# Optimization experiments

Measured on AMD Instinct MI355X. Metric: run time of the kernel, lower is better.

## Reference

```python
import jax, jax.numpy as jnp
import numpy as np

VOL = 128
FACTOR = 0.5 * VOL
N = 262144
LAT = 16
B = 8


def setup_inputs() -> dict:
    key = jax.random.key(0)
    ks = jax.random.split(key, 10)
    x = jax.random.normal(ks[0], (B, LAT), jnp.float32)
    inds = jax.random.randint(ks[1], (N, 3), 1, 126, dtype=jnp.int32)
    reference_values = jax.random.normal(ks[2], (N,), jnp.float32)
    # SIREN first layer: U(-1/in, 1/in)
    W0 = jax.random.uniform(ks[3], (LAT, 8), jnp.float32, -1.0 / LAT, 1.0 / LAT)
    b0 = jnp.zeros((8,), jnp.float32)
    # SIREN hidden layers (4 residual layers): U(-sqrt(6/in), sqrt(6/in))
    lim_h = float(np.sqrt(6.0 / 8.0))
    Wh = jax.random.uniform(ks[4], (4, 8, 8), jnp.float32, -lim_h, lim_h)
    bh = jnp.zeros((4, 8), jnp.float32)
    # final glorot-uniform layer: 8 -> 4N
    lim_f = float(np.sqrt(6.0 / (8.0 + 4.0 * N)))
    Wf = jax.random.uniform(ks[5], (8, 4 * N), jnp.float32, -lim_f, lim_f)
    bf = jnp.zeros((4 * N,), jnp.float32)
    return {"x": x, "W0": W0, "b0": b0, "Wh": Wh, "bh": bh, "Wf": Wf,
            "bf": bf, "reference_values": reference_values, "inds": inds}


def _siren_mlp(x, W0, b0, Wh, bh, Wf, bf):
    bf16 = jnp.bfloat16
    h = jnp.sin(30.0 * (x.astype(bf16) @ W0.astype(bf16) + b0.astype(bf16)))
    for i in range(Wh.shape[0]):  # 4 residual sine layers, 8-wide
        h = h + jnp.sin(h @ Wh[i].astype(bf16) + bh[i].astype(bf16))
    return h.astype(jnp.float32) @ Wf + bf  # [B, 4N], final layer in fp32


def reference(x, W0, b0, Wh, bh, Wf, bf, reference_values, inds):
    Bn = x.shape[0]
    out = _siren_mlp(x, W0, b0, Wh, bh, Wf, bf).reshape(Bn, N, 4)
    delta_coords, delta_values = out[..., :3], out[..., 3]
    # coords = stack(z,y,x reversed) normalized to [-1,1)
    coords_norm = (jnp.stack([inds[:, 2], inds[:, 1], inds[:, 0]], axis=1)
                   .astype(jnp.float32) - FACTOR) / FACTOR  # [N,3]
    values = reference_values + delta_values                 # [B,N]
    coords = FACTOR * (coords_norm[None] + delta_coords) + FACTOR  # [B,N,3]
    bposf = jnp.floor(coords)
    bposi = bposf.astype(jnp.int32)
    f = coords - bposf
    fx, fy, fz = f[..., 0], f[..., 1], f[..., 2]
    gx, gy, gz = 1.0 - fx, 1.0 - fy, 1.0 - fz
    # 8 trilinear weights, in the original concat order
    w = jnp.stack([gx * gy * gz, fx * gy * gz, gx * fy * gz, gx * gy * fz,
                   gx * fy * fz, fx * gy * fz, fx * fy * gz, fx * fy * fz],
                  axis=1)                                    # [B,8,N]
    bamp = (values[:, None, :] * w).reshape(Bn, 8 * N)
    offs = jnp.array([[0, 0, 0], [1, 0, 0], [0, 1, 0], [0, 0, 1],
                      [0, 1, 1], [1, 0, 1], [1, 1, 0], [1, 1, 1]], jnp.int32)
    bpos = (bposi[:, None, :, :] + offs[None, :, None, :]).reshape(Bn, 8 * N, 3)

    def scatter(pos, amp):
        return jnp.zeros((VOL, VOL, VOL), jnp.float32).at[
            pos[:, 2], pos[:, 1], pos[:, 0]].add(amp)

    grids = jax.vmap(scatter)(bpos, bamp)  # [B,128,128,128]
    return grids
```

## Files before the change

kernel.cpp:

```cpp
#include <hip/hip_runtime.h>
#include <math.h>

#define VOL   128
#define V2    (VOL*VOL)
#define V3    (VOL*VOL*VOL)
#define NPTS  262144
#define LATD  16
#define BATCH 8
#define FACTORF 64.0f
#define NBINS (VOL*VOL)
#define RZ 8
#define RY 8
#define NREG_TOTAL 2048
#define REGION_WGS 1280
#define FAR_CAP 8192

#define WS_HBUF    0u
#define WS_HIST    256u
#define WS_START   65792u
#define WS_RANK    131344u
#define WS_KEYS    1179920u
#define WS_CTRL    1704208u
#define WS_FARLIST 1704240u
#define WS_COORDS  1737008u
#define WS_FULL    35291440u

__device__ __forceinline__ float bf16r(float x) {
    unsigned u = __float_as_uint(x);
    u = (u + 0x7fffu + ((u >> 16) & 1u)) & 0xffff0000u;
    return __uint_as_float(u);
}

__global__ void mlp_kernel(const float* __restrict__ x,
                           const float* __restrict__ W0,
                           const float* __restrict__ b0,
                           const float* __restrict__ Wh,
                           const float* __restrict__ bh,
                           float* __restrict__ hout) {
    int b = threadIdx.x;
    if (b >= BATCH) return;
    float xb[LATD];
    #pragma unroll
    for (int i = 0; i < LATD; ++i) xb[i] = bf16r(x[b*LATD + i]);
    float h[8];
    #pragma unroll
    for (int j = 0; j < 8; ++j) {
        float acc = 0.f;
        #pragma unroll
        for (int i = 0; i < LATD; ++i) acc += xb[i] * bf16r(W0[i*8 + j]);
        float t = bf16r(acc);
        t = bf16r(t + bf16r(b0[j]));
        t = bf16r(30.0f * t);
        h[j] = bf16r(sinf(t));
    }
    for (int l = 0; l < 4; ++l) {
        float nh[8];
        #pragma unroll
        for (int j = 0; j < 8; ++j) {
            float acc = 0.f;
            #pragma unroll
            for (int r = 0; r < 8; ++r) acc += h[r] * bf16r(Wh[(l*8 + r)*8 + j]);
            float t = bf16r(acc);
            t = bf16r(t + bf16r(bh[l*8 + j]));
            float s = bf16r(sinf(t));
            nh[j] = bf16r(h[j] + s);
        }
        #pragma unroll
        for (int j = 0; j < 8; ++j) h[j] = nh[j];
    }
    #pragma unroll
    for (int j = 0; j < 8; ++j) hout[b*8 + j] = h[j];
}

__global__ __launch_bounds__(256) void hist_rank_kernel(const int* __restrict__ inds,
                                                        unsigned* __restrict__ hist,
                                                        unsigned* __restrict__ rank) {
    int n = blockIdx.x * 256 + threadIdx.x;
    if (n >= NPTS) return;
    rank[n] = atomicAdd(&hist[inds[n*3]*VOL + inds[n*3+1]], 1u);
}

__global__ __launch_bounds__(256) void scan_kernel(const unsigned* __restrict__ hist,
                                                   unsigned* __restrict__ binstart,
                                                   unsigned* __restrict__ ctrl) {
    __shared__ unsigned part[256];
    int t = threadIdx.x;
    const int CH = NBINS / 256;
    unsigned s = 0;
    for (int k = 0; k < CH; ++k) s += hist[t*CH + k];
    part[t] = s; __syncthreads();
    for (int off = 1; off < 256; off <<= 1) {
        unsigned v = (t >= off) ? part[t - off] : 0u;
        __syncthreads();
        part[t] += v;
        __syncthreads();
    }
    unsigned run = (t == 0) ? 0u : part[t - 1];
    for (int k = 0; k < CH; ++k) {
        int idx = t*CH + k;
        binstart[idx] = run;
        run += hist[idx];
    }
    if (t == 0) { binstart[NBINS] = NPTS; ctrl[0] = 0u; ctrl[1] = 0u; }
}

__global__ __launch_bounds__(256) void coords_kernel(
    const float* __restrict__ Wf, const float* __restrict__ bfv_g,
    const float* __restrict__ rv, const int* __restrict__ inds,
    const float* __restrict__ hbuf, const unsigned* __restrict__ binstart,
    const unsigned* __restrict__ rank, unsigned short* __restrict__ keys,
    unsigned* __restrict__ ctrl, unsigned* __restrict__ farlist,
    float4* __restrict__ coords_s)
{
    __shared__ float hs[64];
    if (threadIdx.x < 64) hs[threadIdx.x] = hbuf[threadIdx.x];
    __syncthreads();
    int n = blockIdx.x * 256 + threadIdx.x;
    if (n >= NPTS) return;
    int iz = inds[n*3], iy = inds[n*3+1], ix = inds[n*3+2];
    float cnx = ((float)ix - FACTORF) / FACTORF;
    float cny = ((float)iy - FACTORF) / FACTORF;
    float cnz = ((float)iz - FACTORF) / FACTORF;
    float val0 = rv[n];
    float4 bfv = ((const float4*)bfv_g)[n];
    float4 wf[8];
    #pragma unroll
    for (int r = 0; r < 8; ++r)
        wf[r] = ((const float4*)(Wf + (size_t)r * 4 * NPTS))[n];
    unsigned pos = binstart[iz*VOL + iy] + rank[n];
    keys[pos] = (unsigned short)((iz << 7) | iy);
    #pragma unroll
    for (int b = 0; b < BATCH; ++b) {
        float o0 = bfv.x, o1 = bfv.y, o2 = bfv.z, o3 = bfv.w;
        #pragma unroll
        for (int r = 0; r < 8; ++r) {
            float hv = hs[b*8 + r];
            o0 = fmaf(hv, wf[r].x, o0);
            o1 = fmaf(hv, wf[r].y, o1);
            o2 = fmaf(hv, wf[r].z, o2);
            o3 = fmaf(hv, wf[r].w, o3);
        }
        float4 c;
        c.x = FACTORF * (cnx + o0) + FACTORF;
        c.y = FACTORF * (cny + o1) + FACTORF;
        c.z = FACTORF * (cnz + o2) + FACTORF;
        c.w = val0 + o3;
        coords_s[(size_t)b * NPTS + pos] = c;
        int bz = (int)floorf(c.z), by = (int)floorf(c.y);
        bool nearzy = ((unsigned)(bz - iz + 2) <= 4u) &&
                      ((unsigned)(by - iy + 2) <= 4u);
        if (!nearzy) {
            unsigned fp = atomicAdd(&ctrl[0], 1u);
            if (fp < FAR_CAP) farlist[fp] = (pos << 3) | (unsigned)b;
        }
    }
}

__global__ __launch_bounds__(256) void region_kernel(
    const float4* __restrict__ coords_s, const unsigned short* __restrict__ keys,
    const unsigned* __restrict__ binstart, unsigned* __restrict__ ctrl,
    float* __restrict__ out)
{
    __shared__ float tile[RZ*RY*VOL];
    __shared__ int reg_s;
    int tid = threadIdx.x;

    const int ox[8] = {0,1,0,0,0,1,1,1};
    const int oy[8] = {0,0,1,0,1,0,1,1};
    const int oz[8] = {0,0,0,1,1,1,0,1};

    for (;;) {
        __syncthreads();
        if (tid == 0) reg_s = (int)atomicAdd(&ctrl[1], 1u);
        __syncthreads();
        int reg = reg_s;
        if (reg >= NREG_TOTAL) return;
        int b   = reg >> 8;
        int rid = reg & 255;
        int z0 = (rid >> 4) * RZ, y0 = (rid & 15) * RY;

        for (int i = tid; i < RZ*RY*VOL; i += 256) tile[i] = 0.f;
        __syncthreads();

        int ylo = y0 - 3, yhi = y0 + RY + 2;
        int sA0, sA1, sB0, sB1;
        if (ylo < 0)        { sA0 = ylo + VOL; sA1 = VOL; sB0 = 0; sB1 = yhi; }
        else if (yhi > VOL) { sA0 = ylo; sA1 = VOL; sB0 = 0; sB1 = yhi - VOL; }
        else                { sA0 = ylo; sA1 = yhi; sB0 = 0; sB1 = 0; }

        const float4* cb = coords_s + (size_t)b * NPTS;

        for (int zr = z0 - 3; zr < z0 + RZ + 2; ++zr) {
            int zz = (zr + VOL) & (VOL-1);
            int base = zz * VOL;
            for (int sg = 0; sg < 2; ++sg) {
                int a  = sg ? sB0 : sA0;
                int e2 = sg ? sB1 : sA1;
                if (a >= e2) continue;
                unsigned s = binstart[base + a];
                unsigned e = binstart[base + e2];
                for (unsigned i = s + tid; i < e; i += 256) {
                    unsigned kv = keys[i];
                    int piz = (int)(kv >> 7), piy = (int)(kv & 127);
                    float4 c = cb[i];
                    float fxf = floorf(c.x), fyf = floorf(c.y), fzf = floorf(c.z);
                    int bx = (int)fxf, by = (int)fyf, bz = (int)fzf;
                    bool nearzy = ((unsigned)(bz - piz + 2) <= 4u) &&
                                  ((unsigned)(by - piy + 2) <= 4u);
                    if (!nearzy) continue;
                    float fx = c.x - fxf, fy = c.y - fyf, fz = c.z - fzf;
                    float gx = 1.f - fx, gy = 1.f - fy, gz = 1.f - fz;
                    float val = c.w;
                    float w[8] = {gx*gy*gz, fx*gy*gz, gx*fy*gz, gx*gy*fz,
                                  gx*fy*fz, fx*gy*fz, fx*fy*gz, fx*fy*fz};
                    #pragma unroll
                    for (int o = 0; o < 8; ++o) {
                        int Z = (bz + oz[o]) & 127, dz = Z - z0;
                        if ((unsigned)dz >= RZ) continue;
                        int Y = (by + oy[o]) & 127, dy = Y - y0;
                        if ((unsigned)dy >= RY) continue;
                        int X = (bx + ox[o]) & 127;
                        atomicAdd(&tile[(dz << 10) + (dy << 7) + X], val * w[o]);
                    }
                }
            }
        }
        __syncthreads();
        size_t ob = (size_t)b * V3;
        for (int i = tid; i < RZ*RY*VOL; i += 256) {
            int lz = i >> 10, ly = (i >> 7) & (RY-1), lx = i & 127;
            out[ob + (size_t)(z0+lz)*V2 + (y0+ly)*VOL + lx] = tile[i];
        }
    }
}

__global__ __launch_bounds__(256) void far_kernel(
    const float4* __restrict__ coords_s, const unsigned* __restrict__ ctrl,
    const unsigned* __restrict__ farlist, float* __restrict__ out)
{
    unsigned cnt = ctrl[0];
    if (cnt > FAR_CAP) cnt = FAR_CAP;
    const int ox[8] = {0,1,0,0,0,1,1,1};
    const int oy[8] = {0,0,1,0,1,0,1,1};
    const int oz[8] = {0,0,0,1,1,1,0,1};
    for (unsigned idx = blockIdx.x * 256 + threadIdx.x; idx < cnt;
         idx += gridDim.x * 256) {
        unsigned e = farlist[idx];
        unsigned pos = e >> 3;
        int b = (int)(e & 7u);
        float4 c = coords_s[(size_t)b * NPTS + pos];
        float fxf = floorf(c.x), fyf = floorf(c.y), fzf = floorf(c.z);
        int bx = (int)fxf, by = (int)fyf, bz = (int)fzf;
        float fx = c.x - fxf, fy = c.y - fyf, fz = c.z - fzf;
        float gx = 1.f - fx, gy = 1.f - fy, gz = 1.f - fz;
        float val = c.w;
        float w[8] = {gx*gy*gz, fx*gy*gz, gx*fy*gz, gx*gy*fz,
                      gx*fy*fz, fx*gy*fz, fx*fy*gz, fx*fy*fz};
        float* ob = out + (size_t)b * V3;
        #pragma unroll
        for (int o = 0; o < 8; ++o) {
            int Z = (bz + oz[o]) & 127;
            int Y = (by + oy[o]) & 127;
            int X = (bx + ox[o]) & 127;
            atomicAdd(ob + (size_t)Z*V2 + Y*VOL + X, val * w[o]);
        }
    }
}

__global__ __launch_bounds__(256) void scatter_fallback(
    const float* __restrict__ Wf, const float* __restrict__ bfv_g,
    const float* __restrict__ rv, const int* __restrict__ inds,
    const float* __restrict__ hbuf, float* __restrict__ out)
{
    __shared__ float hs[BATCH*8];
    if (threadIdx.x < BATCH*8) hs[threadIdx.x] = hbuf[threadIdx.x];
    __syncthreads();
    int n = blockIdx.x * blockDim.x + threadIdx.x;
    if (n >= NPTS) return;
    int iz = inds[n*3 + 0], iy = inds[n*3 + 1], ix = inds[n*3 + 2];
    float cnx = ((float)ix - FACTORF) / FACTORF;
    float cny = ((float)iy - FACTORF) / FACTORF;
    float cnz = ((float)iz - FACTORF) / FACTORF;
    float val0 = rv[n];
    float4 bfv = ((const float4*)bfv_g)[n];
    float4 wf[8];
    #pragma unroll
    for (int r = 0; r < 8; ++r)
        wf[r] = ((const float4*)(Wf + (size_t)r * 4 * NPTS))[n];
    static const int offs[8][3] = {{0,0,0},{1,0,0},{0,1,0},{0,0,1},
                                   {0,1,1},{1,0,1},{1,1,0},{1,1,1}};
    #pragma unroll
    for (int b = 0; b < BATCH; ++b) {
        float o0 = bfv.x, o1 = bfv.y, o2 = bfv.z, o3 = bfv.w;
        #pragma unroll
        for (int r = 0; r < 8; ++r) {
            float hv = hs[b*8 + r];
            o0 = fmaf(hv, wf[r].x, o0);
            o1 = fmaf(hv, wf[r].y, o1);
            o2 = fmaf(hv, wf[r].z, o2);
            o3 = fmaf(hv, wf[r].w, o3);
        }
        float cx = FACTORF * (cnx + o0) + FACTORF;
        float cy = FACTORF * (cny + o1) + FACTORF;
        float cz = FACTORF * (cnz + o2) + FACTORF;
        float val = val0 + o3;
        float fxf = floorf(cx), fyf = floorf(cy), fzf = floorf(cz);
        int bx = (int)fxf, by = (int)fyf, bz = (int)fzf;
        float fx = cx - fxf, fy = cy - fyf, fz = cz - fzf;
        float gx = 1.f - fx, gy = 1.f - fy, gz = 1.f - fz;
        float w[8] = {gx*gy*gz, fx*gy*gz, gx*fy*gz, gx*gy*fz,
                      gx*fy*fz, fx*gy*fz, fx*fy*gz, fx*fy*fz};
        float* ob = out + (size_t)b * V3;
        #pragma unroll
        for (int o = 0; o < 8; ++o) {
            int X = (bx + offs[o][0]) & (VOL-1);
            int Y = (by + offs[o][1]) & (VOL-1);
            int Z = (bz + offs[o][2]) & (VOL-1);
            atomicAdd(ob + (size_t)Z*V2 + Y*VOL + X, val * w[o]);
        }
    }
}

extern "C" void kernel_launch(void* const* d_in, const int* in_sizes, int n_in,
                              void* d_out, int out_size, void* d_ws, size_t ws_size,
                              hipStream_t stream) {
    const float* x    = (const float*)d_in[0];
    const float* W0   = (const float*)d_in[1];
    const float* b0   = (const float*)d_in[2];
    const float* Wh   = (const float*)d_in[3];
    const float* bh   = (const float*)d_in[4];
    const float* Wf   = (const float*)d_in[5];
    const float* bf   = (const float*)d_in[6];
    const float* rv   = (const float*)d_in[7];
    const int*   inds = (const int*)d_in[8];
    float* out = (float*)d_out;
    char*  ws  = (char*)d_ws;

    float*          hbuf     = (float*)(ws + WS_HBUF);
    unsigned*       hist     = (unsigned*)(ws + WS_HIST);
    unsigned*       binstart = (unsigned*)(ws + WS_START);
    unsigned*       rank     = (unsigned*)(ws + WS_RANK);
    unsigned short* keys     = (unsigned short*)(ws + WS_KEYS);
    unsigned*       ctrl     = (unsigned*)(ws + WS_CTRL);
    unsigned*       farlist  = (unsigned*)(ws + WS_FARLIST);
    float4*         coords_s = (float4*)(ws + WS_COORDS);

    mlp_kernel<<<1, 64, 0, stream>>>(x, W0, b0, Wh, bh, hbuf);

    if (ws_size >= (size_t)WS_FULL) {
        hipMemsetAsync(hist, 0, NBINS*4, stream);
        hist_rank_kernel<<<NPTS/256, 256, 0, stream>>>(inds, hist, rank);
        scan_kernel<<<1, 256, 0, stream>>>(hist, binstart, ctrl);
        coords_kernel<<<NPTS/256, 256, 0, stream>>>(Wf, bf, rv, inds, hbuf,
                                                    binstart, rank, keys,
                                                    ctrl, farlist, coords_s);
        region_kernel<<<REGION_WGS, 256, 0, stream>>>(coords_s, keys, binstart,
                                                      ctrl, out);
        far_kernel<<<8, 256, 0, stream>>>(coords_s, ctrl, farlist, out);
    } else {
        hipMemsetAsync(d_out, 0, (size_t)out_size * sizeof(float), stream);
        scatter_fallback<<<NPTS/256, 256, 0, stream>>>(Wf, bf, rv, inds, hbuf, out);
    }
}
```

Baseline: 200.8 us.

## Use static one-region-per-block grid with flattened segment loop and unrolled loads

Replaces the persistent atomic work-queue region kernel with one workgroup per smaller region (RY halved to 4), launching 4096 blocks. Each block precomputes the 26 bin segments of its halo into shared memory and walks them as one flattened index space, issuing four independent loads per thread before the scatter arithmetic. This is meant to remove per-segment loop overhead and idle lanes on short segments, and to raise memory-level parallelism and occupancy. In exchange the halo overlap per block grows, so more points are read and filtered redundantly.

```diff
diff --git a/kernel.cpp b/kernel.cpp
--- a/kernel.cpp
+++ b/kernel.cpp
@@ -10,9 +10,8 @@
 #define FACTORF 64.0f
 #define NBINS (VOL*VOL)
 #define RZ 8
-#define RY 8
-#define NREG_TOTAL 2048
-#define REGION_WGS 1280
+#define RY 4
+#define REG_PER_B ((VOL/RZ)*(VOL/RY))
 #define FAR_CAP 8192
 
 #define WS_HBUF    0u
@@ -158,79 +157,93 @@
 
 __global__ __launch_bounds__(256) void region_kernel(
     const float4* __restrict__ coords_s, const unsigned short* __restrict__ keys,
-    const unsigned* __restrict__ binstart, unsigned* __restrict__ ctrl,
-    float* __restrict__ out)
+    const unsigned* __restrict__ binstart, float* __restrict__ out)
 {
     __shared__ float tile[RZ*RY*VOL];
-    __shared__ int reg_s;
+    __shared__ unsigned rstart[26], rcnt[26], rcum[27];
     int tid = threadIdx.x;
+    int b   = blockIdx.x >> 9;
+    int rid = blockIdx.x & (REG_PER_B - 1);
+    int z0 = (rid >> 5) * RZ, y0 = (rid & 31) * RY;
+
+    for (int i = tid; i < RZ*RY*VOL; i += 256) tile[i] = 0.f;
+
+    if (tid < 13) {
+        int zr = z0 - 3 + tid;
+        int zz = (zr + VOL) & (VOL-1);
+        int base = zz * VOL;
+        int ylo = y0 - 3, yhi = y0 + RY + 2;
+        int a0, a1, b0, b1;
+        if (ylo < 0)        { a0 = ylo + VOL; a1 = VOL; b0 = 0; b1 = yhi; }
+        else if (yhi > VOL) { a0 = ylo; a1 = VOL; b0 = 0; b1 = yhi - VOL; }
+        else                { a0 = ylo; a1 = yhi; b0 = 0; b1 = 0; }
+        unsigned sA = binstart[base + a0];
+        rstart[tid*2]   = sA;
+        rcnt[tid*2]     = binstart[base + a1] - sA;
+        unsigned sB = binstart[base + b0];
+        rstart[tid*2+1] = sB;
+        rcnt[tid*2+1]   = (b1 > b0) ? (binstart[base + b1] - sB) : 0u;
+    }
+    __syncthreads();
+    if (tid == 0) {
+        unsigned run = 0;
+        #pragma unroll
+        for (int r = 0; r < 26; ++r) { rcum[r] = run; run += rcnt[r]; }
+        rcum[26] = run;
+    }
+    __syncthreads();
 
     const int ox[8] = {0,1,0,0,0,1,1,1};
     const int oy[8] = {0,0,1,0,1,0,1,1};
     const int oz[8] = {0,0,0,1,1,1,0,1};
-
-    for (;;) {
-        __syncthreads();
-        if (tid == 0) reg_s = (int)atomicAdd(&ctrl[1], 1u);
-        __syncthreads();
-        int reg = reg_s;
-        if (reg >= NREG_TOTAL) return;
-        int b   = reg >> 8;
-        int rid = reg & 255;
-        int z0 = (rid >> 4) * RZ, y0 = (rid & 15) * RY;
-
-        for (int i = tid; i < RZ*RY*VOL; i += 256) tile[i] = 0.f;
-        __syncthreads();
-
-        int ylo = y0 - 3, yhi = y0 + RY + 2;
-        int sA0, sA1, sB0, sB1;
-        if (ylo < 0)        { sA0 = ylo + VOL; sA1 = VOL; sB0 = 0; sB1 = yhi; }
-        else if (yhi > VOL) { sA0 = ylo; sA1 = VOL; sB0 = 0; sB1 = yhi - VOL; }
-        else                { sA0 = ylo; sA1 = yhi; sB0 = 0; sB1 = 0; }
-
-        const float4* cb = coords_s + (size_t)b * NPTS;
-
-        for (int zr = z0 - 3; zr < z0 + RZ + 2; ++zr) {
-            int zz = (zr + VOL) & (VOL-1);
-            int base = zz * VOL;
-            for (int sg = 0; sg < 2; ++sg) {
-                int a  = sg ? sB0 : sA0;
-                int e2 = sg ? sB1 : sA1;
-                if (a >= e2) continue;
-                unsigned s = binstart[base + a];
-                unsigned e = binstart[base + e2];
-                for (unsigned i = s + tid; i < e; i += 256) {
-                    unsigned kv = keys[i];
-                    int piz = (int)(kv >> 7), piy = (int)(kv & 127);
-                    float4 c = cb[i];
-                    float fxf = floorf(c.x), fyf = floorf(c.y), fzf = floorf(c.z);
-                    int bx = (int)fxf, by = (int)fyf, bz = (int)fzf;
-                    bool nearzy = ((unsigned)(bz - piz + 2) <= 4u) &&
-                                  ((unsigned)(by - piy + 2) <= 4u);
-                    if (!nearzy) continue;
-                    float fx = c.x - fxf, fy = c.y - fyf, fz = c.z - fzf;
-                    float gx = 1.f - fx, gy = 1.f - fy, gz = 1.f - fz;
-                    float val = c.w;
-                    float w[8] = {gx*gy*gz, fx*gy*gz, gx*fy*gz, gx*gy*fz,
-                                  gx*fy*fz, fx*gy*fz, fx*fy*gz, fx*fy*fz};
-                    #pragma unroll
-                    for (int o = 0; o < 8; ++o) {
-                        int Z = (bz + oz[o]) & 127, dz = Z - z0;
-                        if ((unsigned)dz >= RZ) continue;
-                        int Y = (by + oy[o]) & 127, dy = Y - y0;
-                        if ((unsigned)dy >= RY) continue;
-                        int X = (bx + ox[o]) & 127;
-                        atomicAdd(&tile[(dz << 10) + (dy << 7) + X], val * w[o]);
-                    }
-                }
+    const float4* cb = coords_s + (size_t)b * NPTS;
+
+    unsigned total = rcum[26];
+    int r = 0;
+    for (unsigned f = tid; f < total; f += 1024) {
+        float4 c[4]; unsigned kk[4]; bool v[4];
+        #pragma unroll
+        for (int u = 0; u < 4; ++u) {
+            unsigned fu = f + (unsigned)u * 256u;
+            v[u] = fu < total;
+            if (v[u]) {
+                while (fu >= rcum[r+1]) ++r;
+                unsigned j = rstart[r] + (fu - rcum[r]);
+                c[u]  = cb[j];
+                kk[u] = keys[j];
             }
         }
-        __syncthreads();
-        size_t ob = (size_t)b * V3;
-        for (int i = tid; i < RZ*RY*VOL; i += 256) {
-            int lz = i >> 10, ly = (i >> 7) & (RY-1), lx = i & 127;
-            out[ob + (size_t)(z0+lz)*V2 + (y0+ly)*VOL + lx] = tile[i];
-        }
+        #pragma unroll
+        for (int u = 0; u < 4; ++u) {
+            if (!v[u]) continue;
+            int piz = (int)(kk[u] >> 7), piy = (int)(kk[u] & 127u);
+            float4 cc = c[u];
+            float fxf = floorf(cc.x), fyf = floorf(cc.y), fzf = floorf(cc.z);
+            int bx = (int)fxf, by = (int)fyf, bz = (int)fzf;
+            bool nearzy = ((unsigned)(bz - piz + 2) <= 4u) &&
+                          ((unsigned)(by - piy + 2) <= 4u);
+            if (!nearzy) continue;
+            float fx = cc.x - fxf, fy = cc.y - fyf, fz = cc.z - fzf;
+            float gx = 1.f - fx, gy = 1.f - fy, gz = 1.f - fz;
+            float val = cc.w;
+            float w[8] = {gx*gy*gz, fx*gy*gz, gx*fy*gz, gx*gy*fz,
+                          gx*fy*fz, fx*gy*fz, fx*fy*gz, fx*fy*fz};
+            #pragma unroll
+            for (int o = 0; o < 8; ++o) {
+                int Z = (bz + oz[o]) & 127, dz = Z - z0;
+                if ((unsigned)dz >= RZ) continue;
+                int Y = (by + oy[o]) & 127, dy = Y - y0;
+                if ((unsigned)dy >= RY) continue;
+                int X = (bx + ox[o]) & 127;
+                atomicAdd(&tile[(dz << 9) + (dy << 7) + X], val * w[o]);
+            }
+        }
+    }
+    __syncthreads();
+    size_t ob = (size_t)b * V3;
+    for (int i = tid; i < RZ*RY*VOL; i += 256) {
+        int lz = i >> 9, ly = (i >> 7) & (RY-1), lx = i & 127;
+        out[ob + (size_t)(z0+lz)*V2 + (y0+ly)*VOL + lx] = tile[i];
     }
 }
 
@@ -354,8 +367,8 @@
         coords_kernel<<<NPTS/256, 256, 0, stream>>>(Wf, bf, rv, inds, hbuf,
                                                     binstart, rank, keys,
                                                     ctrl, farlist, coords_s);
-        region_kernel<<<REGION_WGS, 256, 0, stream>>>(coords_s, keys, binstart,
-                                                      ctrl, out);
+        region_kernel<<<REG_PER_B*BATCH, 256, 0, stream>>>(coords_s, keys,
+                                                           binstart, out);
         far_kernel<<<8, 256, 0, stream>>>(coords_s, ctrl, farlist, out);
     } else {
         hipMemsetAsync(d_out, 0, (size_t)out_size * sizeof(float), stream);
```

Result: faster. 179.9 us (-10.4%).

## Compress sorted per-point coords to fixed-point ushort4 and flatten region scheduling

Applied to the files above, without the earlier changes.

The coords kernel now stores each near point as a 64-bit record: fixed-point x, y and z offsets relative to the point's bin, plus an fp16 value. This replaces the float4 record and the separate keys array. Far points are written as full float4 records into a dedicated buffer, with the batch index folded into z. The region kernel drops its atomic work-queue for a static one-block-per-region grid. Each block builds a shared-memory index table over its 13x13 halo bins and processes eight points per thread per iteration to raise memory-level parallelism. This roughly halves intermediate traffic but adds quantisation error in coordinates (1/256 in x) and in values (fp16), which may break accuracy tolerance.

```diff
diff --git a/kernel.cpp b/kernel.cpp
--- a/kernel.cpp
+++ b/kernel.cpp
@@ -1,5 +1,7 @@
 #include <hip/hip_runtime.h>
+#include <hip/hip_fp16.h>
 #include <math.h>
+#include <string.h>
 
 #define VOL   128
 #define V2    (VOL*VOL)
@@ -11,24 +13,33 @@
 #define NBINS (VOL*VOL)
 #define RZ 8
 #define RY 8
-#define NREG_TOTAL 2048
-#define REGION_WGS 1280
+#define HALO 13
+#define NRANGE (HALO*HALO)
+#define TBL_CAP 4096
 #define FAR_CAP 8192
 
-#define WS_HBUF    0u
-#define WS_HIST    256u
-#define WS_START   65792u
-#define WS_RANK    131344u
-#define WS_KEYS    1179920u
-#define WS_CTRL    1704208u
-#define WS_FARLIST 1704240u
-#define WS_COORDS  1737008u
-#define WS_FULL    35291440u
+#define WS_HBUF   0u
+#define WS_HIST   256u
+#define WS_START  65792u
+#define WS_RANK   131344u
+#define WS_CTRL   1179920u
+#define WS_FARBUF 1179952u
+#define WS_COORDC 1311024u
+#define WS_FULL   18088240u
 
 __device__ __forceinline__ float bf16r(float x) {
     unsigned u = __float_as_uint(x);
     u = (u + 0x7fffu + ((u >> 16) & 1u)) & 0xffff0000u;
     return __uint_as_float(u);
+}
+__device__ __forceinline__ unsigned short f16bits(float v) {
+    __half h = __float2half_rn(v);
+    unsigned short us; memcpy(&us, &h, 2);
+    return us;
+}
+__device__ __forceinline__ float f16val(unsigned short us) {
+    __half h; memcpy(&h, &us, 2);
+    return __half2float(h);
 }
 
 __global__ void mlp_kernel(const float* __restrict__ x,
@@ -108,9 +119,9 @@
     const float* __restrict__ Wf, const float* __restrict__ bfv_g,
     const float* __restrict__ rv, const int* __restrict__ inds,
     const float* __restrict__ hbuf, const unsigned* __restrict__ binstart,
-    const unsigned* __restrict__ rank, unsigned short* __restrict__ keys,
-    unsigned* __restrict__ ctrl, unsigned* __restrict__ farlist,
-    float4* __restrict__ coords_s)
+    const unsigned* __restrict__ rank,
+    unsigned* __restrict__ ctrl, float4* __restrict__ farbuf,
+    ushort4* __restrict__ coords_c)
 {
     __shared__ float hs[64];
     if (threadIdx.x < 64) hs[threadIdx.x] = hbuf[threadIdx.x];
@@ -128,7 +139,6 @@
     for (int r = 0; r < 8; ++r)
         wf[r] = ((const float4*)(Wf + (size_t)r * 4 * NPTS))[n];
     unsigned pos = binstart[iz*VOL + iy] + rank[n];
-    keys[pos] = (unsigned short)((iz << 7) | iy);
     #pragma unroll
     for (int b = 0; b < BATCH; ++b) {
         float o0 = bfv.x, o1 = bfv.y, o2 = bfv.z, o3 = bfv.w;
@@ -140,103 +150,135 @@
             o2 = fmaf(hv, wf[r].z, o2);
             o3 = fmaf(hv, wf[r].w, o3);
         }
-        float4 c;
-        c.x = FACTORF * (cnx + o0) + FACTORF;
-        c.y = FACTORF * (cny + o1) + FACTORF;
-        c.z = FACTORF * (cnz + o2) + FACTORF;
-        c.w = val0 + o3;
-        coords_s[(size_t)b * NPTS + pos] = c;
-        int bz = (int)floorf(c.z), by = (int)floorf(c.y);
+        float cx = FACTORF * (cnx + o0) + FACTORF;
+        float cy = FACTORF * (cny + o1) + FACTORF;
+        float cz = FACTORF * (cnz + o2) + FACTORF;
+        float val = val0 + o3;
+        int bz = (int)floorf(cz), by = (int)floorf(cy);
         bool nearzy = ((unsigned)(bz - iz + 2) <= 4u) &&
                       ((unsigned)(by - iy + 2) <= 4u);
-        if (!nearzy) {
+        ushort4 e;
+        if (nearzy) {
+            e.x = (unsigned short)fminf(fmaxf(fmaf(cx + 8.f, 256.f, 0.5f), 0.f), 65535.f);
+            e.y = (unsigned short)fminf(fmaf(cy - (float)iy + 2.f, 8192.f, 0.5f), 40959.f);
+            e.z = (unsigned short)fminf(fmaf(cz - (float)iz + 2.f, 8192.f, 0.5f), 40959.f);
+            e.w = f16bits(val);
+        } else {
+            e.x = 0; e.y = 0xFFFFu; e.z = 0; e.w = 0;
             unsigned fp = atomicAdd(&ctrl[0], 1u);
-            if (fp < FAR_CAP) farlist[fp] = (pos << 3) | (unsigned)b;
-        }
+            if (fp < FAR_CAP)
+                farbuf[fp] = make_float4(cx, cy, cz + 256.0f * (float)b, val);
+        }
+        coords_c[(size_t)b * NPTS + pos] = e;
     }
 }
 
 __global__ __launch_bounds__(256) void region_kernel(
-    const float4* __restrict__ coords_s, const unsigned short* __restrict__ keys,
-    const unsigned* __restrict__ binstart, unsigned* __restrict__ ctrl,
-    float* __restrict__ out)
+    const ushort4* __restrict__ coords_c,
+    const unsigned* __restrict__ binstart, float* __restrict__ out)
 {
     __shared__ float tile[RZ*RY*VOL];
-    __shared__ int reg_s;
+    __shared__ unsigned tbl[TBL_CAP];
+    __shared__ unsigned rcum[NRANGE+1];
+    __shared__ int rbase[NRANGE];
     int tid = threadIdx.x;
-
+    int b   = blockIdx.x >> 8;
+    int rid = blockIdx.x & 255;
+    int z0 = (rid >> 4) * RZ, y0 = (rid & 15) * RY;
+
+    for (int i = tid; i < RZ*RY*VOL; i += 256) tile[i] = 0.f;
+
+    unsigned rs = 0;
+    if (tid < NRANGE) {
+        int zi = tid / HALO, yi = tid - zi * HALO;
+        int zz = (z0 - 3 + zi) & (VOL-1);
+        int yy = (y0 - 3 + yi) & (VOL-1);
+        int base = zz * VOL + yy;
+        rs = binstart[base];
+        rcum[tid+1] = binstart[base+1] - rs;
+    }
+    if (tid == 0) rcum[0] = 0u;
+    __syncthreads();
+    for (int off = 1; off < NRANGE; off <<= 1) {
+        unsigned v = 0u;
+        if (tid < NRANGE && tid >= off) v = rcum[tid+1-off];
+        __syncthreads();
+        if (tid < NRANGE && tid >= off) rcum[tid+1] += v;
+        __syncthreads();
+    }
+    if (tid < NRANGE) rbase[tid] = (int)rs - (int)rcum[tid];
+    __syncthreads();
+
+    unsigned total = rcum[NRANGE];
+    const ushort4* cb = coords_c + (size_t)b * NPTS;
     const int ox[8] = {0,1,0,0,0,1,1,1};
     const int oy[8] = {0,0,1,0,1,0,1,1};
     const int oz[8] = {0,0,0,1,1,1,0,1};
 
-    for (;;) {
-        __syncthreads();
-        if (tid == 0) reg_s = (int)atomicAdd(&ctrl[1], 1u);
-        __syncthreads();
-        int reg = reg_s;
-        if (reg >= NREG_TOTAL) return;
-        int b   = reg >> 8;
-        int rid = reg & 255;
-        int z0 = (rid >> 4) * RZ, y0 = (rid & 15) * RY;
-
-        for (int i = tid; i < RZ*RY*VOL; i += 256) tile[i] = 0.f;
-        __syncthreads();
-
-        int ylo = y0 - 3, yhi = y0 + RY + 2;
-        int sA0, sA1, sB0, sB1;
-        if (ylo < 0)        { sA0 = ylo + VOL; sA1 = VOL; sB0 = 0; sB1 = yhi; }
-        else if (yhi > VOL) { sA0 = ylo; sA1 = VOL; sB0 = 0; sB1 = yhi - VOL; }
-        else                { sA0 = ylo; sA1 = yhi; sB0 = 0; sB1 = 0; }
-
-        const float4* cb = coords_s + (size_t)b * NPTS;
-
-        for (int zr = z0 - 3; zr < z0 + RZ + 2; ++zr) {
-            int zz = (zr + VOL) & (VOL-1);
-            int base = zz * VOL;
-            for (int sg = 0; sg < 2; ++sg) {
-                int a  = sg ? sB0 : sA0;
-                int e2 = sg ? sB1 : sA1;
-                if (a >= e2) continue;
-                unsigned s = binstart[base + a];
-                unsigned e = binstart[base + e2];
-                for (unsigned i = s + tid; i < e; i += 256) {
-                    unsigned kv = keys[i];
-                    int piz = (int)(kv >> 7), piy = (int)(kv & 127);
-                    float4 c = cb[i];
-                    float fxf = floorf(c.x), fyf = floorf(c.y), fzf = floorf(c.z);
-                    int bx = (int)fxf, by = (int)fyf, bz = (int)fzf;
-                    bool nearzy = ((unsigned)(bz - piz + 2) <= 4u) &&
-                                  ((unsigned)(by - piy + 2) <= 4u);
-                    if (!nearzy) continue;
-                    float fx = c.x - fxf, fy = c.y - fyf, fz = c.z - fzf;
-                    float gx = 1.f - fx, gy = 1.f - fy, gz = 1.f - fz;
-                    float val = c.w;
-                    float w[8] = {gx*gy*gz, fx*gy*gz, gx*fy*gz, gx*gy*fz,
-                                  gx*fy*fz, fx*gy*fz, fx*fy*gz, fx*fy*fz};
-                    #pragma unroll
-                    for (int o = 0; o < 8; ++o) {
-                        int Z = (bz + oz[o]) & 127, dz = Z - z0;
-                        if ((unsigned)dz >= RZ) continue;
-                        int Y = (by + oy[o]) & 127, dy = Y - y0;
-                        if ((unsigned)dy >= RY) continue;
-                        int X = (bx + ox[o]) & 127;
-                        atomicAdd(&tile[(dz << 10) + (dy << 7) + X], val * w[o]);
-                    }
+    for (unsigned c0 = 0; c0 < total; c0 += TBL_CAP) {
+        unsigned c1 = (total - c0 < TBL_CAP) ? total : c0 + TBL_CAP;
+        __syncthreads();
+        if (tid < NRANGE) {
+            unsigned lo = rcum[tid] > c0 ? rcum[tid] : c0;
+            unsigned hi = rcum[tid+1] < c1 ? rcum[tid+1] : c1;
+            int zi = tid / HALO, yi = tid - zi * HALO;
+            unsigned meta = ((unsigned)zi << 22) | ((unsigned)yi << 26);
+            int rb = rbase[tid];
+            for (unsigned i = lo; i < hi; ++i)
+                tbl[i - c0] = (unsigned)(rb + (int)i) | meta;
+        }
+        __syncthreads();
+        unsigned nn = c1 - c0;
+        for (unsigned f = tid; f < nn; f += 2048u) {
+            ushort4 e[8]; unsigned t[8]; bool v[8];
+            #pragma unroll
+            for (int u = 0; u < 8; ++u) {
+                unsigned fu = f + (unsigned)u * 256u;
+                v[u] = fu < nn;
+                if (v[u]) {
+                    t[u] = tbl[fu];
+                    e[u] = cb[t[u] & 0x3FFFFFu];
                 }
             }
-        }
-        __syncthreads();
-        size_t ob = (size_t)b * V3;
-        for (int i = tid; i < RZ*RY*VOL; i += 256) {
-            int lz = i >> 10, ly = (i >> 7) & (RY-1), lx = i & 127;
-            out[ob + (size_t)(z0+lz)*V2 + (y0+ly)*VOL + lx] = tile[i];
-        }
+            #pragma unroll
+            for (int u = 0; u < 8; ++u) {
+                if (!v[u] || e[u].y == 0xFFFFu) continue;
+                int zi = (int)((t[u] >> 22) & 15u), yi = (int)((t[u] >> 26) & 15u);
+                int piz = (z0 - 3 + zi) & (VOL-1);
+                int piy = (y0 - 3 + yi) & (VOL-1);
+                float cx = (float)e[u].x * (1.f/256.f) - 8.f;
+                float cy = (float)piy + (float)e[u].y * (1.f/8192.f) - 2.f;
+                float cz = (float)piz + (float)e[u].z * (1.f/8192.f) - 2.f;
+                float val = f16val(e[u].w);
+                float fxf = floorf(cx), fyf = floorf(cy), fzf = floorf(cz);
+                int bx = (int)fxf, by = (int)fyf, bz = (int)fzf;
+                float fx = cx - fxf, fy = cy - fyf, fz = cz - fzf;
+                float gx = 1.f - fx, gy = 1.f - fy, gz = 1.f - fz;
+                float w[8] = {gx*gy*gz, fx*gy*gz, gx*fy*gz, gx*gy*fz,
+                              gx*fy*fz, fx*gy*fz, fx*fy*gz, fx*fy*fz};
+                #pragma unroll
+                for (int o = 0; o < 8; ++o) {
+                    int Z = (bz + oz[o]) & (VOL-1), dz = Z - z0;
+                    if ((unsigned)dz >= RZ) continue;
+                    int Y = (by + oy[o]) & (VOL-1), dy = Y - y0;
+                    if ((unsigned)dy >= RY) continue;
+                    int X = (bx + ox[o]) & (VOL-1);
+                    atomicAdd(&tile[(dz << 10) + (dy << 7) + X], val * w[o]);
+                }
+            }
+        }
+    }
+    __syncthreads();
+    size_t ob = (size_t)b * V3;
+    for (int i = tid; i < RZ*RY*VOL; i += 256) {
+        int lz = i >> 10, ly = (i >> 7) & (RY-1), lx = i & 127;
+        out[ob + (size_t)(z0+lz)*V2 + (y0+ly)*VOL + lx] = tile[i];
     }
 }
 
 __global__ __launch_bounds__(256) void far_kernel(
-    const float4* __restrict__ coords_s, const unsigned* __restrict__ ctrl,
-    const unsigned* __restrict__ farlist, float* __restrict__ out)
+    const unsigned* __restrict__ ctrl, const float4* __restrict__ farbuf,
+    float* __restrict__ out)
 {
     unsigned cnt = ctrl[0];
     if (cnt > FAR_CAP) cnt = FAR_CAP;
@@ -245,13 +287,12 @@
     const int oz[8] = {0,0,0,1,1,1,0,1};
     for (unsigned idx = blockIdx.x * 256 + threadIdx.x; idx < cnt;
          idx += gridDim.x * 256) {
-        unsigned e = farlist[idx];
-        unsigned pos = e >> 3;
-        int b = (int)(e & 7u);
-        float4 c = coords_s[(size_t)b * NPTS + pos];
-        float fxf = floorf(c.x), fyf = floorf(c.y), fzf = floorf(c.z);
+        float4 c = farbuf[idx];
+        int b = (int)floorf((c.z + 8.0f) * (1.0f/256.0f));
+        float cz = c.z - 256.0f * (float)b;
+        float fxf = floorf(c.x), fyf = floorf(c.y), fzf = floorf(cz);
         int bx = (int)fxf, by = (int)fyf, bz = (int)fzf;
-        float fx = c.x - fxf, fy = c.y - fyf, fz = c.z - fzf;
+        float fx = c.x - fxf, fy = c.y - fyf, fz = cz - fzf;
         float gx = 1.f - fx, gy = 1.f - fy, gz = 1.f - fz;
         float val = c.w;
         float w[8] = {gx*gy*gz, fx*gy*gz, gx*fy*gz, gx*gy*fz,
@@ -259,9 +300,9 @@
         float* ob = out + (size_t)b * V3;
         #pragma unroll
         for (int o = 0; o < 8; ++o) {
-            int Z = (bz + oz[o]) & 127;
-            int Y = (by + oy[o]) & 127;
-            int X = (bx + ox[o]) & 127;
+            int Z = (bz + oz[o]) & (VOL-1);
+            int Y = (by + oy[o]) & (VOL-1);
+            int X = (bx + ox[o]) & (VOL-1);
             atomicAdd(ob + (size_t)Z*V2 + Y*VOL + X, val * w[o]);
         }
     }
@@ -336,14 +377,13 @@
     float* out = (float*)d_out;
     char*  ws  = (char*)d_ws;
 
-    float*          hbuf     = (float*)(ws + WS_HBUF);
-    unsigned*       hist     = (unsigned*)(ws + WS_HIST);
-    unsigned*       binstart = (unsigned*)(ws + WS_START);
-    unsigned*       rank     = (unsigned*)(ws + WS_RANK);
-    unsigned short* keys     = (unsigned short*)(ws + WS_KEYS);
-    unsigned*       ctrl     = (unsigned*)(ws + WS_CTRL);
-    unsigned*       farlist  = (unsigned*)(ws + WS_FARLIST);
-    float4*         coords_s = (float4*)(ws + WS_COORDS);
+    float*    hbuf     = (float*)(ws + WS_HBUF);
+    unsigned* hist     = (unsigned*)(ws + WS_HIST);
+    unsigned* binstart = (unsigned*)(ws + WS_START);
+    unsigned* rank     = (unsigned*)(ws + WS_RANK);
+    unsigned* ctrl     = (unsigned*)(ws + WS_CTRL);
+    float4*   farbuf   = (float4*)(ws + WS_FARBUF);
+    ushort4*  coords_c = (ushort4*)(ws + WS_COORDC);
 
     mlp_kernel<<<1, 64, 0, stream>>>(x, W0, b0, Wh, bh, hbuf);
 
@@ -352,11 +392,10 @@
         hist_rank_kernel<<<NPTS/256, 256, 0, stream>>>(inds, hist, rank);
         scan_kernel<<<1, 256, 0, stream>>>(hist, binstart, ctrl);
         coords_kernel<<<NPTS/256, 256, 0, stream>>>(Wf, bf, rv, inds, hbuf,
-                                                    binstart, rank, keys,
-                                                    ctrl, farlist, coords_s);
-        region_kernel<<<REGION_WGS, 256, 0, stream>>>(coords_s, keys, binstart,
-                                                      ctrl, out);
-        far_kernel<<<8, 256, 0, stream>>>(coords_s, ctrl, farlist, out);
+                                                    binstart, rank,
+                                                    ctrl, farbuf, coords_c);
+        region_kernel<<<256*BATCH, 256, 0, stream>>>(coords_c, binstart, out);
+        far_kernel<<<8, 256, 0, stream>>>(ctrl, farbuf, out);
     } else {
         hipMemsetAsync(d_out, 0, (size_t)out_size * sizeof(float), stream);
         scatter_fallback<<<NPTS/256, 256, 0, stream>>>(Wf, bf, rv, inds, hbuf, out);
```

New measurement: 188.1 us. -6.3%, faster.
